# Performance work log

Hardware: AMD Instinct MI355X
Metric: run time of the kernel (lower is better)

The kernel has to match this reference:

```python
import jax, jax.numpy as jnp
import numpy as np

N_NODES = 50000
N_EDGES = 800000
IN_CH, HID_CH, OUT_CH = 256, 128, 64


def setup_inputs() -> dict:
    key = jax.random.key(0)
    k_x, k_e, k_w1, k_w2 = jax.random.split(key, 4)
    x = jax.random.normal(k_x, (N_NODES, IN_CH), dtype=jnp.float32)
    edge_index = jax.random.randint(k_e, (2, N_EDGES), 0, N_NODES, dtype=jnp.int32)
    # Glorot-style init like PyG GCNConv (weight [in, out], bias zeros)
    s1 = float(np.sqrt(6.0 / (IN_CH + HID_CH)))
    s2 = float(np.sqrt(6.0 / (HID_CH + OUT_CH)))
    W1 = jax.random.uniform(k_w1, (IN_CH, HID_CH), jnp.float32, -s1, s1)
    b1 = jnp.zeros((HID_CH,), jnp.float32)
    W2 = jax.random.uniform(k_w2, (HID_CH, OUT_CH), jnp.float32, -s2, s2)
    b2 = jnp.zeros((OUT_CH,), jnp.float32)
    return {"x": x, "edge_index": edge_index, "W1": W1, "b1": b1, "W2": W2, "b2": b2}


def _gcn_conv(x, src, dst, deg_inv_sqrt, W, b, n_nodes):
    """GCNConv with self-loops: D^{-1/2}(A+I)D^{-1/2} X W + b."""
    h = x @ W  # [N, out]
    norm = deg_inv_sqrt[src] * deg_inv_sqrt[dst]          # [E]
    msgs = h[src] * norm[:, None]                          # [E, out] gather
    agg = jax.ops.segment_sum(msgs, dst, num_segments=n_nodes)  # scatter-add
    self_loop = h * (deg_inv_sqrt * deg_inv_sqrt)[:, None]      # self-loop term
    return agg + self_loop + b


def reference(x, edge_index, W1, b1, W2, b2):
    n = x.shape[0]
    src, dst = edge_index[0], edge_index[1]
    # degree includes self-loop (+1), edge weight 1, counted at destination
    deg = jnp.zeros((n,), x.dtype).at[dst].add(1.0) + 1.0
    dis = jax.lax.rsqrt(deg)
    h = jax.nn.relu(_gcn_conv(x, src, dst, dis, W1, b1, n))
    out = jax.nn.relu(_gcn_conv(h, src, dst, dis, W2, b2, n))
    return out
```

## Files before the change

### kernel.cpp

```cpp
#include <hip/hip_runtime.h>

#define N_NODES 50000
#define N_EDGES 800000
#define IN_CH 256
#define HID_CH 128
#define OUT_CH 64
#define CAP 80

typedef _Float16 f16;
typedef _Float16 f16x8 __attribute__((ext_vector_type(8)));
typedef _Float16 f16x2 __attribute__((ext_vector_type(2)));
typedef float f32x4 __attribute__((ext_vector_type(4)));

__global__ __launch_bounds__(256) void k_fill(const int* __restrict__ src,
                                              const int* __restrict__ dst,
                                              int* __restrict__ cnt,
                                              int* __restrict__ bucket, int E) {
    int e = blockIdx.x * 256 + threadIdx.x;
    if (e < E) {
        int d = dst[e];
        int pos = atomicAdd(&cnt[d], 1);
        if (pos < CAP) bucket[(size_t)d * CAP + pos] = src[e];
    }
}

__global__ __launch_bounds__(256) void k_dis(const int* __restrict__ cnt,
                                             float* __restrict__ dis, int N) {
    int i = blockIdx.x * 256 + threadIdx.x;
    if (i < N) dis[i] = rsqrtf((float)cnt[i] + 1.0f);
}

template <int K, int N>
__global__ __launch_bounds__(256) void k_swizzleB(const float* __restrict__ W,
                                                  f16* __restrict__ Bsw) {
    constexpr int NTILES = N / 16;
    int idx = blockIdx.x * 256 + threadIdx.x;
    if (idx >= K * N) return;
    int j = idx & 7;
    int lane = (idx >> 3) & 63;
    int rest = idx >> 9;
    int nt = rest % NTILES;
    int ks = rest / NTILES;
    int k = ks * 32 + (lane >> 4) * 8 + j;
    int n = nt * 16 + (lane & 15);
    Bsw[idx] = (f16)W[(size_t)k * N + n];
}

template <int K, int N, bool A_FP32, bool RELU>
__global__ __launch_bounds__(256) void k_gemm(const void* __restrict__ Av,
                                              const f16* __restrict__ Bsw,
                                              const float* __restrict__ dis,
                                              f16* __restrict__ C, int M) {
    constexpr int KSTEPS = K / 32, NTILES = N / 16;
    const int tid = threadIdx.x;
    const int wave = tid >> 6, lane = tid & 63;
    const int quad = lane >> 4, l16 = lane & 15;
    int row = blockIdx.x * 64 + wave * 16 + l16;
    const int rowc = row < M ? row : M - 1;

    f32x4 acc[NTILES];
#pragma unroll
    for (int t = 0; t < NTILES; ++t) acc[t] = (f32x4){0.f, 0.f, 0.f, 0.f};

#pragma unroll
    for (int ks = 0; ks < KSTEPS; ++ks) {
        f16x8 afrag;
        if (A_FP32) {
            const float* A = (const float*)Av;
            const float4* p = (const float4*)(A + (size_t)rowc * K + ks * 32 + quad * 8);
            float4 v0 = p[0], v1 = p[1];
            afrag[0] = (f16)v0.x; afrag[1] = (f16)v0.y;
            afrag[2] = (f16)v0.z; afrag[3] = (f16)v0.w;
            afrag[4] = (f16)v1.x; afrag[5] = (f16)v1.y;
            afrag[6] = (f16)v1.z; afrag[7] = (f16)v1.w;
        } else {
            const f16* A = (const f16*)Av;
            afrag = *(const f16x8*)(A + (size_t)rowc * K + ks * 32 + quad * 8);
            if (RELU) {
#pragma unroll
                for (int j = 0; j < 8; ++j)
                    afrag[j] = afrag[j] > (f16)0 ? afrag[j] : (f16)0;
            }
        }
#pragma unroll
        for (int t = 0; t < NTILES; ++t) {
            f16x8 bfrag = *(const f16x8*)(Bsw + (((size_t)ks * NTILES + t) * 64 + lane) * 8);
            acc[t] = __builtin_amdgcn_mfma_f32_16x16x32_f16(afrag, bfrag, acc[t], 0, 0, 0);
        }
    }

    int rbase = blockIdx.x * 64 + wave * 16 + quad * 4;
#pragma unroll
    for (int r = 0; r < 4; ++r) {
        int gr = rbase + r;
        if (gr < M) {
            float d = dis[gr];
#pragma unroll
            for (int t = 0; t < NTILES; ++t)
                C[(size_t)gr * N + t * 16 + l16] = (f16)(acc[t][r] * d);
        }
    }
}

template <int C, bool RELU_OUT_F32>
__global__ __launch_bounds__(256) void k_pull(const f16* __restrict__ g,
                                              const float* __restrict__ dis,
                                              const float* __restrict__ bias,
                                              const int* __restrict__ cnt,
                                              const int* __restrict__ bucket,
                                              void* __restrict__ outv, int N) {
    constexpr int LPN = C / 2;
    int tid = blockIdx.x * 256 + threadIdx.x;
    int u = tid / LPN;
    int sub = tid % LPN;
    if (u >= N) return;

    f16x2 hv = *(const f16x2*)(g + (size_t)u * C + sub * 2);
    float a0 = (float)hv[0];
    float a1 = (float)hv[1];

    int n = cnt[u];
    if (n > CAP) n = CAP;
    const int* row = bucket + (size_t)u * CAP;

    int k = 0;
    for (; k + 4 <= n; k += 4) {
        int4 s4 = *(const int4*)(row + k);
        f16x2 v0 = *(const f16x2*)(g + (size_t)s4.x * C + sub * 2);
        f16x2 v1 = *(const f16x2*)(g + (size_t)s4.y * C + sub * 2);
        f16x2 v2 = *(const f16x2*)(g + (size_t)s4.z * C + sub * 2);
        f16x2 v3 = *(const f16x2*)(g + (size_t)s4.w * C + sub * 2);
        a0 += (float)v0[0] + (float)v1[0] + (float)v2[0] + (float)v3[0];
        a1 += (float)v0[1] + (float)v1[1] + (float)v2[1] + (float)v3[1];
    }
    for (; k < n; ++k) {
        int s = row[k];
        f16x2 v = *(const f16x2*)(g + (size_t)s * C + sub * 2);
        a0 += (float)v[0];
        a1 += (float)v[1];
    }

    float du = dis[u];
    float o0 = fmaf(du, a0, bias[sub * 2]);
    float o1 = fmaf(du, a1, bias[sub * 2 + 1]);
    if (RELU_OUT_F32) {
        float2* out = (float2*)outv;
        out[(size_t)u * LPN + sub] = make_float2(fmaxf(o0, 0.f), fmaxf(o1, 0.f));
    } else {
        f16x2 o;
        o[0] = (f16)o0; o[1] = (f16)o1;
        *(f16x2*)((f16*)outv + (size_t)u * C + sub * 2) = o;
    }
}


extern "C" void kernel_launch(void* const* d_in, const int* in_sizes, int n_in,
                              void* d_out, int out_size, void* d_ws, size_t ws_size,
                              hipStream_t stream) {
    const float* x  = (const float*)d_in[0];
    const int* ei   = (const int*)d_in[1];
    const float* W1 = (const float*)d_in[2];
    const float* b1 = (const float*)d_in[3];
    const float* W2 = (const float*)d_in[4];
    const float* b2 = (const float*)d_in[5];
    float* out = (float*)d_out;

    const int* src = ei;
    const int* dst = ei + N_EDGES;

    char* ws = (char*)d_ws;
    size_t off = 0;
    auto alloc = [&](size_t bytes) -> void* {
        off = (off + 255) & ~(size_t)255;
        void* p = ws + off;
        off += bytes;
        return p;
    };
    int*   cnt    = (int*)alloc((size_t)N_NODES * 4);
    float* dis    = (float*)alloc((size_t)N_NODES * 4);
    int*   bucket = (int*)alloc((size_t)N_NODES * CAP * 4);
    f16*   W1sw   = (f16*)alloc((size_t)IN_CH * HID_CH * 2);
    f16*   W2sw   = (f16*)alloc((size_t)HID_CH * OUT_CH * 2);
    f16*   g1     = (f16*)alloc((size_t)N_NODES * HID_CH * 2);
    f16*   agg1   = (f16*)alloc((size_t)N_NODES * HID_CH * 2);
    f16*   g2     = (f16*)alloc((size_t)N_NODES * OUT_CH * 2);

    hipMemsetAsync(cnt, 0, (size_t)N_NODES * 4, stream);
    k_fill<<<(N_EDGES + 255) / 256, 256, 0, stream>>>(src, dst, cnt, bucket, N_EDGES);
    k_dis<<<(N_NODES + 255) / 256, 256, 0, stream>>>(cnt, dis, N_NODES);
    k_swizzleB<IN_CH, HID_CH><<<(IN_CH * HID_CH + 255) / 256, 256, 0, stream>>>(W1, W1sw);
    k_swizzleB<HID_CH, OUT_CH><<<(HID_CH * OUT_CH + 255) / 256, 256, 0, stream>>>(W2, W2sw);

    k_gemm<IN_CH, HID_CH, true, false><<<(N_NODES + 63) / 64, 256, 0, stream>>>(x, W1sw, dis, g1, N_NODES);
    k_pull<HID_CH, false><<<(N_NODES * (HID_CH / 2) + 255) / 256, 256, 0, stream>>>(
        g1, dis, b1, cnt, bucket, agg1, N_NODES);

    k_gemm<HID_CH, OUT_CH, false, true><<<(N_NODES + 63) / 64, 256, 0, stream>>>(agg1, W2sw, dis, g2, N_NODES);
    k_pull<OUT_CH, true><<<(N_NODES * (OUT_CH / 2) + 255) / 256, 256, 0, stream>>>(
        g2, dis, b2, cnt, bucket, out, N_NODES);
}
```

Measured before the change: 231.8 us.

## Build adjacency via binned counting sort in cooperative kernel; widen pull gathers

Replaces the global-atomic bucket fill with a three-phase binned counting sort (histogram, placement, per-bin local bucket build in LDS) fused into one cooperative kernel with grid syncs, with weight swizzles folded in and a non-cooperative fallback. Bucket indices are stored as 16-bit with CAP reduced to 64, and the pull kernels now gather 8 halfs per lane with 8-way unrolled neighbour loads. This aims to cut global atomic contention, launch count and index bandwidth, at the risk of dropping edges for nodes with more than 64 in-neighbours and relying on node ids fitting in 16 bits. Edge order within buckets now depends on atomic ordering.

Result: slower. 318.5 us (+37.4%).

```diff
diff --git a/kernel.cpp b/kernel.cpp
--- a/kernel.cpp
+++ b/kernel.cpp
@@ -1,41 +1,30 @@
 #include <hip/hip_runtime.h>
+#include <hip/hip_cooperative_groups.h>
+
+namespace cg = cooperative_groups;
 
 #define N_NODES 50000
 #define N_EDGES 800000
 #define IN_CH 256
 #define HID_CH 128
 #define OUT_CH 64
-#define CAP 80
+#define CAP 64
+#define NBINS 196
+#define CBLOCKS 256
+#define CCHUNK 3125
+#define SWZ_ELEMS (IN_CH * HID_CH + HID_CH * OUT_CH)
 
 typedef _Float16 f16;
 typedef _Float16 f16x8 __attribute__((ext_vector_type(8)));
-typedef _Float16 f16x2 __attribute__((ext_vector_type(2)));
 typedef float f32x4 __attribute__((ext_vector_type(4)));
-
-__global__ __launch_bounds__(256) void k_fill(const int* __restrict__ src,
-                                              const int* __restrict__ dst,
-                                              int* __restrict__ cnt,
-                                              int* __restrict__ bucket, int E) {
-    int e = blockIdx.x * 256 + threadIdx.x;
-    if (e < E) {
-        int d = dst[e];
-        int pos = atomicAdd(&cnt[d], 1);
-        if (pos < CAP) bucket[(size_t)d * CAP + pos] = src[e];
-    }
-}
-
-__global__ __launch_bounds__(256) void k_dis(const int* __restrict__ cnt,
-                                             float* __restrict__ dis, int N) {
-    int i = blockIdx.x * 256 + threadIdx.x;
-    if (i < N) dis[i] = rsqrtf((float)cnt[i] + 1.0f);
-}
+typedef unsigned short u16;
+typedef unsigned int u32;
+
 
 template <int K, int N>
-__global__ __launch_bounds__(256) void k_swizzleB(const float* __restrict__ W,
-                                                  f16* __restrict__ Bsw) {
+__device__ __forceinline__ void swz(const float* __restrict__ W, f16* __restrict__ Bsw,
+                                    int idx) {
     constexpr int NTILES = N / 16;
-    int idx = blockIdx.x * 256 + threadIdx.x;
-    if (idx >= K * N) return;
     int j = idx & 7;
     int lane = (idx >> 3) & 63;
     int rest = idx >> 9;
@@ -44,6 +33,163 @@
     int k = ks * 32 + (lane >> 4) * 8 + j;
     int n = nt * 16 + (lane & 15);
     Bsw[idx] = (f16)W[(size_t)k * N + n];
+}
+
+__device__ __forceinline__ void swz_all(int idx, const float* __restrict__ W1,
+                                        const float* __restrict__ W2,
+                                        f16* __restrict__ W1sw, f16* __restrict__ W2sw) {
+    if (idx < IN_CH * HID_CH) swz<IN_CH, HID_CH>(W1, W1sw, idx);
+    else if (idx < SWZ_ELEMS) swz<HID_CH, OUT_CH>(W2, W2sw, idx - IN_CH * HID_CH);
+}
+
+__device__ __forceinline__ void hist_body(int b, const int* __restrict__ dst,
+                                          int* __restrict__ binCnt, int* lcnt) {
+    const int tid = threadIdx.x;
+    for (int i = tid; i < NBINS; i += 256) lcnt[i] = 0;
+    __syncthreads();
+    int base = b * CCHUNK;
+    for (int i = tid; i < CCHUNK; i += 256)
+        atomicAdd(&lcnt[dst[base + i] >> 8], 1);
+    __syncthreads();
+    for (int i = tid; i < NBINS; i += 256)
+        if (lcnt[i]) atomicAdd(&binCnt[i], lcnt[i]);
+}
+
+__device__ __forceinline__ void scan_local(const int* __restrict__ binCnt,
+                                           int* sc, int* vv) {
+    const int t = threadIdx.x;
+    int v = (t < NBINS) ? binCnt[t] : 0;
+    sc[t] = v; vv[t] = v;
+    __syncthreads();
+    for (int ofs = 1; ofs < 256; ofs <<= 1) {
+        int add = (t >= ofs) ? sc[t - ofs] : 0;
+        __syncthreads();
+        sc[t] += add;
+        __syncthreads();
+    }
+}
+
+__device__ __forceinline__ void place_body(int b, const int* __restrict__ src,
+                                           const int* __restrict__ dst,
+                                           const int* sc, const int* vv,
+                                           int* __restrict__ binCursor,
+                                           u32* __restrict__ ebuf,
+                                           u32* codes, int* lcnt, int* lbase, int* lcur) {
+    const int tid = threadIdx.x;
+    for (int i = tid; i < NBINS; i += 256) lcnt[i] = 0;
+    __syncthreads();
+    int base = b * CCHUNK;
+    for (int j = tid; j < CCHUNK; j += 256) {
+        u32 d = (u32)dst[base + j];
+        codes[j] = (d << 16) | (u32)src[base + j];
+        atomicAdd(&lcnt[d >> 8], 1);
+    }
+    __syncthreads();
+    for (int i = tid; i < NBINS; i += 256) {
+        lbase[i] = (sc[i] - vv[i]) + atomicAdd(&binCursor[i], lcnt[i]);
+        lcur[i] = 0;
+    }
+    __syncthreads();
+    for (int j = tid; j < CCHUNK; j += 256) {
+        u32 c = codes[j];
+        int bb = c >> 24;
+        int p = atomicAdd(&lcur[bb], 1);
+        ebuf[lbase[bb] + p] = c;
+    }
+}
+
+__device__ __forceinline__ void build_body(int b, const u32* __restrict__ ebuf,
+                                           const int* sc, const int* vv,
+                                           int* __restrict__ cnt, float* __restrict__ dis,
+                                           u16* __restrict__ bucket,
+                                           int* lcnt, u16* lbuck) {
+    const int tid = threadIdx.x;
+    lcnt[tid] = 0;
+    __syncthreads();
+    int s = sc[b] - vv[b], e = sc[b];
+    for (int i = s + tid; i < e; i += 256) {
+        u32 c = ebuf[i];
+        int local = (c >> 16) & 255;
+        int p = atomicAdd(&lcnt[local], 1);
+        if (p < CAP) lbuck[local * CAP + p] = (u16)(c & 0xFFFFu);
+    }
+    __syncthreads();
+    int nodeBase = b << 8;
+    if (nodeBase + tid < N_NODES) {
+        cnt[nodeBase + tid] = lcnt[tid];
+        dis[nodeBase + tid] = rsqrtf((float)lcnt[tid] + 1.0f);
+    }
+    const uint4* ls = (const uint4*)lbuck;
+    uint4* gd = (uint4*)(bucket + (size_t)nodeBase * CAP);
+    for (int idx = tid; idx < 256 * CAP / 8; idx += 256) {
+        int row = idx >> 3;
+        if (nodeBase + row < N_NODES) gd[idx] = ls[idx];
+    }
+}
+
+__global__ __launch_bounds__(256) void k_csr(const int* __restrict__ src,
+                                             const int* __restrict__ dst,
+                                             const float* __restrict__ W1,
+                                             const float* __restrict__ W2,
+                                             int* __restrict__ binCnt,
+                                             int* __restrict__ binCursor,
+                                             u32* __restrict__ ebuf,
+                                             int* __restrict__ cnt,
+                                             float* __restrict__ dis,
+                                             u16* __restrict__ bucket,
+                                             f16* __restrict__ W1sw,
+                                             f16* __restrict__ W2sw) {
+    __shared__ int lcnt[256], sc[256], vv[256], lbase[256], lcur[256];
+    __shared__ __align__(16) char payload[32768];
+    const int bid = blockIdx.x;
+    cg::grid_group grid = cg::this_grid();
+
+    swz_all(bid * 256 + threadIdx.x, W1, W2, W1sw, W2sw);
+    hist_body(bid, dst, binCnt, lcnt);
+    __threadfence();
+    grid.sync();
+
+    scan_local(binCnt, sc, vv);
+    place_body(bid, src, dst, sc, vv, binCursor, ebuf,
+               (u32*)payload, lcnt, lbase, lcur);
+    __threadfence();
+    grid.sync();
+
+    if (bid < NBINS)
+        build_body(bid, ebuf, sc, vv, cnt, dis, bucket, lcnt, (u16*)payload);
+}
+
+__global__ __launch_bounds__(256) void k_hist_sb(const int* __restrict__ dst,
+                                                 int* __restrict__ binCnt,
+                                                 const float* __restrict__ W1,
+                                                 const float* __restrict__ W2,
+                                                 f16* __restrict__ W1sw,
+                                                 f16* __restrict__ W2sw) {
+    __shared__ int lcnt[256];
+    swz_all(blockIdx.x * 256 + threadIdx.x, W1, W2, W1sw, W2sw);
+    hist_body(blockIdx.x, dst, binCnt, lcnt);
+}
+
+__global__ __launch_bounds__(256) void k_place_sb(const int* __restrict__ src,
+                                                  const int* __restrict__ dst,
+                                                  const int* __restrict__ binCnt,
+                                                  int* __restrict__ binCursor,
+                                                  u32* __restrict__ ebuf) {
+    __shared__ int lcnt[256], sc[256], vv[256], lbase[256], lcur[256];
+    __shared__ __align__(16) u32 codes[CCHUNK];
+    scan_local(binCnt, sc, vv);
+    place_body(blockIdx.x, src, dst, sc, vv, binCursor, ebuf, codes, lcnt, lbase, lcur);
+}
+
+__global__ __launch_bounds__(256) void k_build_sb(const u32* __restrict__ ebuf,
+                                                  const int* __restrict__ binCnt,
+                                                  int* __restrict__ cnt,
+                                                  float* __restrict__ dis,
+                                                  u16* __restrict__ bucket) {
+    __shared__ int lcnt[256], sc[256], vv[256];
+    __shared__ __align__(16) u16 lbuck[256 * CAP];
+    scan_local(binCnt, sc, vv);
+    build_body(blockIdx.x, ebuf, sc, vv, cnt, dis, bucket, lcnt, lbuck);
 }
 
 template <int K, int N, bool A_FP32, bool RELU>
@@ -102,55 +248,142 @@
     }
 }
 
-template <int C, bool RELU_OUT_F32>
-__global__ __launch_bounds__(256) void k_pull(const f16* __restrict__ g,
-                                              const float* __restrict__ dis,
-                                              const float* __restrict__ bias,
-                                              const int* __restrict__ cnt,
-                                              const int* __restrict__ bucket,
-                                              void* __restrict__ outv, int N) {
-    constexpr int LPN = C / 2;
-    int tid = blockIdx.x * 256 + threadIdx.x;
-    int u = tid / LPN;
-    int sub = tid % LPN;
-    if (u >= N) return;
-
-    f16x2 hv = *(const f16x2*)(g + (size_t)u * C + sub * 2);
-    float a0 = (float)hv[0];
-    float a1 = (float)hv[1];
+__global__ __launch_bounds__(256) void k_pull1(const f16* __restrict__ g1,
+                                               const float* __restrict__ dis,
+                                               const float* __restrict__ b1,
+                                               const int* __restrict__ cnt,
+                                               const u16* __restrict__ bucket,
+                                               f16* __restrict__ agg1) {
+    int gtid = blockIdx.x * 256 + threadIdx.x;
+    int u = gtid >> 4;
+    int sub = gtid & 15;
+    if (u >= N_NODES) return;
+    const f16* gp = g1 + sub * 8;
+
+    f16x8 sv = *(const f16x8*)(gp + (size_t)u * HID_CH);
+    float a[8];
+#pragma unroll
+    for (int j = 0; j < 8; ++j) a[j] = (float)sv[j];
 
     int n = cnt[u];
     if (n > CAP) n = CAP;
-    const int* row = bucket + (size_t)u * CAP;
+    const u16* row = bucket + u * CAP;
 
     int k = 0;
-    for (; k + 4 <= n; k += 4) {
-        int4 s4 = *(const int4*)(row + k);
-        f16x2 v0 = *(const f16x2*)(g + (size_t)s4.x * C + sub * 2);
-        f16x2 v1 = *(const f16x2*)(g + (size_t)s4.y * C + sub * 2);
-        f16x2 v2 = *(const f16x2*)(g + (size_t)s4.z * C + sub * 2);
-        f16x2 v3 = *(const f16x2*)(g + (size_t)s4.w * C + sub * 2);
-        a0 += (float)v0[0] + (float)v1[0] + (float)v2[0] + (float)v3[0];
-        a1 += (float)v0[1] + (float)v1[1] + (float)v2[1] + (float)v3[1];
+    for (; k + 8 <= n; k += 8) {
+        uint4 iv = *(const uint4*)(row + k);
+        int s0 = iv.x & 0xFFFF, s1 = iv.x >> 16;
+        int s2 = iv.y & 0xFFFF, s3 = iv.y >> 16;
+        int s4 = iv.z & 0xFFFF, s5 = iv.z >> 16;
+        int s6 = iv.w & 0xFFFF, s7 = iv.w >> 16;
+        f16x8 v0 = *(const f16x8*)(gp + (size_t)s0 * HID_CH);
+        f16x8 v1 = *(const f16x8*)(gp + (size_t)s1 * HID_CH);
+        f16x8 v2 = *(const f16x8*)(gp + (size_t)s2 * HID_CH);
+        f16x8 v3 = *(const f16x8*)(gp + (size_t)s3 * HID_CH);
+        f16x8 v4 = *(const f16x8*)(gp + (size_t)s4 * HID_CH);
+        f16x8 v5 = *(const f16x8*)(gp + (size_t)s5 * HID_CH);
+        f16x8 v6 = *(const f16x8*)(gp + (size_t)s6 * HID_CH);
+        f16x8 v7 = *(const f16x8*)(gp + (size_t)s7 * HID_CH);
+#pragma unroll
+        for (int j = 0; j < 8; ++j)
+            a[j] += (((float)v0[j] + (float)v1[j]) + ((float)v2[j] + (float)v3[j])) +
+                    (((float)v4[j] + (float)v5[j]) + ((float)v6[j] + (float)v7[j]));
+    }
+    if (k + 4 <= n) {
+        ushort4 s4v = *(const ushort4*)(row + k);
+        f16x8 v0 = *(const f16x8*)(gp + (size_t)s4v.x * HID_CH);
+        f16x8 v1 = *(const f16x8*)(gp + (size_t)s4v.y * HID_CH);
+        f16x8 v2 = *(const f16x8*)(gp + (size_t)s4v.z * HID_CH);
+        f16x8 v3 = *(const f16x8*)(gp + (size_t)s4v.w * HID_CH);
+#pragma unroll
+        for (int j = 0; j < 8; ++j)
+            a[j] += ((float)v0[j] + (float)v1[j]) + ((float)v2[j] + (float)v3[j]);
+        k += 4;
     }
     for (; k < n; ++k) {
-        int s = row[k];
-        f16x2 v = *(const f16x2*)(g + (size_t)s * C + sub * 2);
-        a0 += (float)v[0];
-        a1 += (float)v[1];
+        f16x8 v = *(const f16x8*)(gp + (size_t)row[k] * HID_CH);
+#pragma unroll
+        for (int j = 0; j < 8; ++j) a[j] += (float)v[j];
     }
 
     float du = dis[u];
-    float o0 = fmaf(du, a0, bias[sub * 2]);
-    float o1 = fmaf(du, a1, bias[sub * 2 + 1]);
-    if (RELU_OUT_F32) {
-        float2* out = (float2*)outv;
-        out[(size_t)u * LPN + sub] = make_float2(fmaxf(o0, 0.f), fmaxf(o1, 0.f));
-    } else {
-        f16x2 o;
-        o[0] = (f16)o0; o[1] = (f16)o1;
-        *(f16x2*)((f16*)outv + (size_t)u * C + sub * 2) = o;
-    }
+    f16x8 o;
+#pragma unroll
+    for (int j = 0; j < 8; ++j) o[j] = (f16)fmaf(du, a[j], b1[sub * 8 + j]);
+    *(f16x8*)(agg1 + (size_t)u * HID_CH + sub * 8) = o;
+}
+
+__global__ __launch_bounds__(256) void k_pull2(const f16* __restrict__ g2,
+                                               const float* __restrict__ dis,
+                                               const float* __restrict__ b2,
+                                               const int* __restrict__ cnt,
+                                               const u16* __restrict__ bucket,
+                                               float* __restrict__ out) {
+    int gtid = blockIdx.x * 256 + threadIdx.x;
+    int u = gtid >> 3;
+    int sub = gtid & 7;
+    if (u >= N_NODES) return;
+    const f16* gp = g2 + sub * 8;
+
+    f16x8 sv = *(const f16x8*)(gp + (size_t)u * OUT_CH);
+    float a[8];
+#pragma unroll
+    for (int j = 0; j < 8; ++j) a[j] = (float)sv[j];
+
+    int n = cnt[u];
+    if (n > CAP) n = CAP;
+    const u16* row = bucket + u * CAP;
+
+    int k = 0;
+    for (; k + 8 <= n; k += 8) {
+        uint4 iv = *(const uint4*)(row + k);
+        int s0 = iv.x & 0xFFFF, s1 = iv.x >> 16;
+        int s2 = iv.y & 0xFFFF, s3 = iv.y >> 16;
+        int s4 = iv.z & 0xFFFF, s5 = iv.z >> 16;
+        int s6 = iv.w & 0xFFFF, s7 = iv.w >> 16;
+        f16x8 v0 = *(const f16x8*)(gp + (size_t)s0 * OUT_CH);
+        f16x8 v1 = *(const f16x8*)(gp + (size_t)s1 * OUT_CH);
+        f16x8 v2 = *(const f16x8*)(gp + (size_t)s2 * OUT_CH);
+        f16x8 v3 = *(const f16x8*)(gp + (size_t)s3 * OUT_CH);
+        f16x8 v4 = *(const f16x8*)(gp + (size_t)s4 * OUT_CH);
+        f16x8 v5 = *(const f16x8*)(gp + (size_t)s5 * OUT_CH);
+        f16x8 v6 = *(const f16x8*)(gp + (size_t)s6 * OUT_CH);
+        f16x8 v7 = *(const f16x8*)(gp + (size_t)s7 * OUT_CH);
+#pragma unroll
+        for (int j = 0; j < 8; ++j)
+            a[j] += (((float)v0[j] + (float)v1[j]) + ((float)v2[j] + (float)v3[j])) +
+                    (((float)v4[j] + (float)v5[j]) + ((float)v6[j] + (float)v7[j]));
+    }
+    if (k + 4 <= n) {
+        ushort4 s4v = *(const ushort4*)(row + k);
+        f16x8 v0 = *(const f16x8*)(gp + (size_t)s4v.x * OUT_CH);
+        f16x8 v1 = *(const f16x8*)(gp + (size_t)s4v.y * OUT_CH);
+        f16x8 v2 = *(const f16x8*)(gp + (size_t)s4v.z * OUT_CH);
+        f16x8 v3 = *(const f16x8*)(gp + (size_t)s4v.w * OUT_CH);
+#pragma unroll
+        for (int j = 0; j < 8; ++j)
+            a[j] += ((float)v0[j] + (float)v1[j]) + ((float)v2[j] + (float)v3[j]);
+        k += 4;
+    }
+    for (; k < n; ++k) {
+        f16x8 v = *(const f16x8*)(gp + (size_t)row[k] * OUT_CH);
+#pragma unroll
+        for (int j = 0; j < 8; ++j) a[j] += (float)v[j];
+    }
+
+    float du = dis[u];
+    float4* op = (float4*)(out + (size_t)u * OUT_CH + sub * 8);
+    float4 o0, o1;
+    o0.x = fmaxf(fmaf(du, a[0], b2[sub * 8 + 0]), 0.f);
+    o0.y = fmaxf(fmaf(du, a[1], b2[sub * 8 + 1]), 0.f);
+    o0.z = fmaxf(fmaf(du, a[2], b2[sub * 8 + 2]), 0.f);
+    o0.w = fmaxf(fmaf(du, a[3], b2[sub * 8 + 3]), 0.f);
+    o1.x = fmaxf(fmaf(du, a[4], b2[sub * 8 + 4]), 0.f);
+    o1.y = fmaxf(fmaf(du, a[5], b2[sub * 8 + 5]), 0.f);
+    o1.z = fmaxf(fmaf(du, a[6], b2[sub * 8 + 6]), 0.f);
+    o1.w = fmaxf(fmaf(du, a[7], b2[sub * 8 + 7]), 0.f);
+    op[0] = o0;
+    op[1] = o1;
 }
 
 
@@ -176,26 +409,41 @@
         off += bytes;
         return p;
     };
+    int*   zbuf   = (int*)alloc((size_t)(NBINS * 2) * 4);
+    int*   binCnt = zbuf;
+    int*   binCursor = zbuf + NBINS;
+    u32*   ebuf   = (u32*)alloc((size_t)N_EDGES * 4);
     int*   cnt    = (int*)alloc((size_t)N_NODES * 4);
     float* dis    = (float*)alloc((size_t)N_NODES * 4);
-    int*   bucket = (int*)alloc((size_t)N_NODES * CAP * 4);
+    u16*   bucket = (u16*)alloc((size_t)N_NODES * CAP * 2);
     f16*   W1sw   = (f16*)alloc((size_t)IN_CH * HID_CH * 2);
     f16*   W2sw   = (f16*)alloc((size_t)HID_CH * OUT_CH * 2);
     f16*   g1     = (f16*)alloc((size_t)N_NODES * HID_CH * 2);
     f16*   agg1   = (f16*)alloc((size_t)N_NODES * HID_CH * 2);
     f16*   g2     = (f16*)alloc((size_t)N_NODES * OUT_CH * 2);
 
-    hipMemsetAsync(cnt, 0, (size_t)N_NODES * 4, stream);
-    k_fill<<<(N_EDGES + 255) / 256, 256, 0, stream>>>(src, dst, cnt, bucket, N_EDGES);
-    k_dis<<<(N_NODES + 255) / 256, 256, 0, stream>>>(cnt, dis, N_NODES);
-    k_swizzleB<IN_CH, HID_CH><<<(IN_CH * HID_CH + 255) / 256, 256, 0, stream>>>(W1, W1sw);
-    k_swizzleB<HID_CH, OUT_CH><<<(HID_CH * OUT_CH + 255) / 256, 256, 0, stream>>>(W2, W2sw);
-
-    k_gemm<IN_CH, HID_CH, true, false><<<(N_NODES + 63) / 64, 256, 0, stream>>>(x, W1sw, dis, g1, N_NODES);
-    k_pull<HID_CH, false><<<(N_NODES * (HID_CH / 2) + 255) / 256, 256, 0, stream>>>(
-        g1, dis, b1, cnt, bucket, agg1, N_NODES);
-
-    k_gemm<HID_CH, OUT_CH, false, true><<<(N_NODES + 63) / 64, 256, 0, stream>>>(agg1, W2sw, dis, g2, N_NODES);
-    k_pull<OUT_CH, true><<<(N_NODES * (OUT_CH / 2) + 255) / 256, 256, 0, stream>>>(
-        g2, dis, b2, cnt, bucket, out, N_NODES);
-}
+    hipMemsetAsync(zbuf, 0, (size_t)(NBINS * 2) * 4, stream);
+
+    void* args[] = {
+        (void*)&src, (void*)&dst, (void*)&W1, (void*)&W2,
+        (void*)&binCnt, (void*)&binCursor, (void*)&ebuf,
+        (void*)&cnt, (void*)&dis, (void*)&bucket, (void*)&W1sw, (void*)&W2sw
+    };
+    hipError_t err = hipLaunchCooperativeKernel((const void*)k_csr, dim3(CBLOCKS),
+                                                dim3(256), args, 0, stream);
+    if (err != hipSuccess) {
+        k_hist_sb<<<CBLOCKS, 256, 0, stream>>>(dst, binCnt, W1, W2, W1sw, W2sw);
+        k_place_sb<<<CBLOCKS, 256, 0, stream>>>(src, dst, binCnt, binCursor, ebuf);
+        k_build_sb<<<NBINS, 256, 0, stream>>>(ebuf, binCnt, cnt, dis, bucket);
+    }
+
+    k_gemm<IN_CH, HID_CH, true, false><<<(N_NODES + 63) / 64, 256, 0, stream>>>(
+        x, W1sw, dis, g1, N_NODES);
+
+    k_pull1<<<(N_NODES * 16 + 255) / 256, 256, 0, stream>>>(g1, dis, b1, cnt, bucket, agg1);
+
+    k_gemm<HID_CH, OUT_CH, false, true><<<(N_NODES + 63) / 64, 256, 0, stream>>>(
+        agg1, W2sw, dis, g2, N_NODES);
+
+    k_pull2<<<(N_NODES * 8 + 255) / 256, 256, 0, stream>>>(g2, dis, b2, cnt, bucket, out);
+}
```
